# Optimization experiments

Hardware: AMD Instinct MI355X
Metric: run time of the kernel (lower is better)

Reference implementation:

```python
import jax, jax.numpy as jnp
import numpy as np

N = 10000
E = 80000
NUM_TYPES = 1000
IN_CH = 64
EMB = 128
IN_GNN = EMB + IN_CH - 1  # 191
NUM_GRAPHS = 16
NUM_CLASSES = 2


def _glorot(key, shape):
    fan_in, fan_out = shape[0], shape[1]
    lim = jnp.sqrt(6.0 / (fan_in + fan_out))
    return jax.random.uniform(key, shape, jnp.float32, -lim, lim)


def setup_inputs() -> dict:
    key = jax.random.key(0)
    ks = jax.random.split(key, 20)
    node_type_ids = jax.random.randint(ks[0], (N,), 0, NUM_TYPES)
    other_feats = jax.random.normal(ks[1], (N, IN_CH - 1), jnp.float32)
    edge_index = jax.random.randint(ks[2], (2, E), 0, N)
    batch = jnp.sort(jax.random.randint(ks[3], (N,), 0, NUM_GRAPHS))
    params = dict(
        emb=jax.random.normal(ks[4], (NUM_TYPES, EMB), jnp.float32),
        W1=_glorot(ks[5], (IN_GNN, 2048)), b1=jnp.zeros((2048,), jnp.float32),
        W2=_glorot(ks[6], (2048, 1024)), b2=jnp.zeros((1024,), jnp.float32),
        W3=_glorot(ks[7], (1024, 1024)), b3=jnp.zeros((1024,), jnp.float32),
        h1w=_glorot(ks[8], (1024, 1024)), h1b=jnp.zeros((1024,), jnp.float32),
        h2w=_glorot(ks[9], (1024, 1024)), h2b=jnp.zeros((1024,), jnp.float32),
        h3w=_glorot(ks[10], (1024, 512)), h3b=jnp.zeros((512,), jnp.float32),
        ow=_glorot(ks[11], (512, NUM_CLASSES)), ob=jnp.zeros((NUM_CLASSES,), jnp.float32),
    )
    return dict(node_type_ids=node_type_ids, other_feats=other_feats,
                edge_index=edge_index, batch=batch, **params)


def _gcn_norm(edge_index, num_nodes):
    # add self loops + symmetric normalization D^-1/2 (A+I) D^-1/2 (PyG GCNConv defaults)
    loop = jnp.arange(num_nodes, dtype=edge_index.dtype)
    src = jnp.concatenate([edge_index[0], loop])
    dst = jnp.concatenate([edge_index[1], loop])
    deg = jax.ops.segment_sum(jnp.ones_like(src, jnp.float32), dst, num_segments=num_nodes)
    dinv = jnp.where(deg > 0, jax.lax.rsqrt(jnp.maximum(deg, 1.0)), 0.0)
    norm = dinv[src] * dinv[dst]
    return src, dst, norm


def _gcn_conv(x, src, dst, norm, W, b):
    h = x @ W                                    # [N, out] dense GEMM first (PyG order)
    msg = h[src] * norm[:, None]                 # gather + scale over edges
    agg = jax.ops.segment_sum(msg, dst, num_segments=x.shape[0])  # scatter-add
    return agg + b


def reference(node_type_ids, other_feats, edge_index, batch,
              emb, W1, b1, W2, b2, W3, b3,
              h1w, h1b, h2w, h2b, h3w, h3b, ow, ob):
    # eval mode: dropout is identity
    x = jnp.concatenate([emb[node_type_ids], other_feats], axis=-1)  # [N, 191]
    src, dst, norm = _gcn_norm(edge_index, x.shape[0])
    x = jax.nn.relu(_gcn_conv(x, src, dst, norm, W1, b1))
    x = jax.nn.relu(_gcn_conv(x, src, dst, norm, W2, b2))
    x = jax.nn.relu(_gcn_conv(x, src, dst, norm, W3, b3))
    # global mean pool over graphs
    sums = jax.ops.segment_sum(x, batch, num_segments=NUM_GRAPHS)
    cnts = jax.ops.segment_sum(jnp.ones((x.shape[0],), jnp.float32), batch, num_segments=NUM_GRAPHS)
    g = sums / jnp.maximum(cnts, 1.0)[:, None]   # [G, 1024]
    g = jax.nn.relu(g @ h1w + h1b)
    g = jax.nn.relu(g @ h2w + h2b)
    g = jax.nn.relu(g @ h3w + h3b)
    return g @ ow + ob                           # [G, num_classes]
```

## Files before the change

### kernel.cpp

```cpp
#include <hip/hip_runtime.h>


#define N_NODES 10000
#define N_EDGES 80000
#define EMB_DIM 128
#define FEAT_DIM 63
#define IN_GNN 191
#define IN_STRIDE 192
#define H1 2048
#define H2 1024
#define NGRAPH 16
#define NCLS 2
#define PCHUNK 8

using ushort = unsigned short;
typedef __attribute__((ext_vector_type(8))) short s8b;
typedef __attribute__((ext_vector_type(4))) float f4v;

__device__ __forceinline__ float us2f(ushort u) {
    union { unsigned int i; float f; } v; v.i = ((unsigned int)u) << 16; return v.f;
}
__device__ __forceinline__ ushort f2us(float f) {
    union { unsigned int i; float f; } v; v.f = f;
    unsigned int r = v.i + 0x7FFFu + ((v.i >> 16) & 1u);
    return (ushort)(r >> 16);
}
__device__ __forceinline__ float ldm(const void* p, long i, int md) {
    return (md == 1) ? us2f(((const ushort*)p)[i]) : ((const float*)p)[i];
}

__global__ void GraphV1EmbLarge_73864847556672_kernel() {}

__global__ void k_detect(const ushort* __restrict__ feats, int* __restrict__ mode) {
    if (threadIdx.x != 0 || blockIdx.x != 0) return;
    int sane = 0;
    for (int i = 0; i < 256; i++) {
        ushort u = feats[i];
        int e = (u >> 7) & 0xFF;
        if (u == 0 || (e >= 97 && e <= 157)) sane++;
    }
    *mode = (sane >= 220) ? 1 : 2;
}

__global__ void k_zero2(int* __restrict__ a, int na, float* __restrict__ b, int nb) {
    int i = blockIdx.x * 256 + threadIdx.x;
    if (i < na) a[i] = 0;
    if (i < nb) b[i] = 0.f;
}
__global__ void k_deg_i(const int* __restrict__ dst, int* __restrict__ cnt) {
    int e = blockIdx.x * blockDim.x + threadIdx.x;
    if (e < N_EDGES) atomicAdd(&cnt[dst[e]], 1);
}
__global__ void k_scan(const int* __restrict__ cnt, int* __restrict__ indptr,
                       float* __restrict__ dinv) {
    __shared__ int part[256];
    int t = threadIdx.x;
    int base = t * 40;
    int s = 0;
    for (int i = 0; i < 40; i++) { int idx = base + i; if (idx < N_NODES) s += cnt[idx]; }
    part[t] = s;
    __syncthreads();
    if (t == 0) {
        int run = 0;
        for (int i = 0; i < 256; i++) { int tmp = part[i]; part[i] = run; run += tmp; }
        indptr[N_NODES] = run;
    }
    __syncthreads();
    int run = part[t];
    for (int i = 0; i < 40; i++) {
        int idx = base + i;
        if (idx < N_NODES) {
            indptr[idx] = run; run += cnt[idx];
            dinv[idx] = rsqrtf((float)cnt[idx] + 1.0f);
        }
    }
}
__global__ void k_fill(const int* __restrict__ src, const int* __restrict__ dst,
                       const int* __restrict__ indptr, int* __restrict__ cursor,
                       const float* __restrict__ dinv, int* __restrict__ ecol,
                       float* __restrict__ ewgt) {
    int e = blockIdx.x * blockDim.x + threadIdx.x;
    if (e >= N_EDGES) return;
    int d = dst[e], s = src[e];
    int slot = indptr[d] + atomicAdd(&cursor[d], 1);
    ecol[slot] = s;
    ewgt[slot] = dinv[s] * dinv[d];
}
__global__ void k_starts(const int* __restrict__ batch, int* __restrict__ starts) {
    int i = blockIdx.x * blockDim.x + threadIdx.x;
    if (i > N_NODES) return;
    int bc = (i < N_NODES) ? batch[i] : NGRAPH;
    int bp = (i == 0) ? -1 : batch[i - 1];
    for (int g = bp + 1; g <= bc; g++) starts[g] = i;
}

__global__ void k_build_x0(const int* __restrict__ types, const void* __restrict__ emb,
                           const void* __restrict__ feats, ushort* __restrict__ x0,
                           const int* __restrict__ mode) {
    int md = *mode;
    int i = blockIdx.x;
    int c = threadIdx.x;
    float v = 0.f;
    if (c < EMB_DIM) v = ldm(emb, (long)types[i] * EMB_DIM + c, md);
    else if (c < IN_GNN) v = ldm(feats, (long)i * FEAT_DIM + (c - EMB_DIM), md);
    x0[(long)i * IN_STRIDE + c] = f2us(v);
}

__device__ __forceinline__ void cvt_tile(const void* W, int K, int N, int Kp,
                                         ushort* Wt, int n0, int k0, int md) {
    __shared__ float tile[32][33];
    int tx = threadIdx.x, ty = threadIdx.y;
    for (int r = ty; r < 32; r += 8) {
        int k = k0 + r;
        tile[r][tx] = (k < K) ? ldm(W, (long)k * N + n0 + tx, md) : 0.f;
    }
    __syncthreads();
    for (int r = ty; r < 32; r += 8) {
        int nn = n0 + r, kk = k0 + tx;
        if (kk < Kp) Wt[(long)nn * Kp + kk] = f2us(tile[tx][r]);
    }
}

__global__ void k_cvtT_all(const void* W1, const void* W2, const void* W3,
                           const void* h1, const void* h2, const void* h3,
                           ushort* W1t, ushort* W2t, ushort* W3t,
                           ushort* h1t, ushort* h2t, ushort* h3t,
                           const int* __restrict__ mode) {
    int md = *mode;
    int b = blockIdx.x;
    if (b < 384) {
        int t = b;        cvt_tile(W1, IN_GNN, H1, IN_STRIDE, W1t, (t % 64) * 32, (t / 64) * 32, md);
    } else if (b < 2432) {
        int t = b - 384;  cvt_tile(W2, H1, H2, H1, W2t, (t % 32) * 32, (t / 32) * 32, md);
    } else if (b < 3456) {
        int t = b - 2432; cvt_tile(W3, H2, H2, H2, W3t, (t % 32) * 32, (t / 32) * 32, md);
    } else if (b < 4480) {
        int t = b - 3456; cvt_tile(h1, H2, H2, H2, h1t, (t % 32) * 32, (t / 32) * 32, md);
    } else if (b < 5504) {
        int t = b - 4480; cvt_tile(h2, H2, H2, H2, h2t, (t % 32) * 32, (t / 32) * 32, md);
    } else {
        int t = b - 5504; cvt_tile(h3, H2, 512, H2, h3t, (t % 16) * 32, (t / 16) * 32, md);
    }
}

__global__ void k_biases(const void* __restrict__ b1, const void* __restrict__ b2,
                         const void* __restrict__ b3, float* __restrict__ b1f,
                         float* __restrict__ b2f, float* __restrict__ b3f,
                         const int* __restrict__ mode) {
    int md = *mode;
    int i = blockIdx.x * 256 + threadIdx.x;
    if (i < 2048) b1f[i] = ldm(b1, i, md);
    else if (i < 3072) b2f[i - 2048] = ldm(b2, (long)(i - 2048), md);
    else if (i < 4096) b3f[i - 3072] = ldm(b3, (long)(i - 3072), md);
}

__global__ void k_gather192(const ushort* __restrict__ H, const int* __restrict__ indptr,
                            const int* __restrict__ ecol, const float* __restrict__ ewgt,
                            const float* __restrict__ dinv, ushort* __restrict__ X) {
    int d = blockIdx.x;
    int c = threadIdx.x;
    float ds = dinv[d];
    float acc = us2f(H[(long)d * IN_STRIDE + c]) * ds * ds;
    int s0 = indptr[d], s1 = indptr[d + 1];
    int s = s0;
    for (; s + 1 < s1; s += 2) {
        int sa = ecol[s], sb = ecol[s + 1];
        float wa = ewgt[s], wb = ewgt[s + 1];
        float fa = us2f(H[(long)sa * IN_STRIDE + c]);
        float fb = us2f(H[(long)sb * IN_STRIDE + c]);
        acc += fa * wa + fb * wb;
    }
    if (s < s1) acc += us2f(H[(long)ecol[s] * IN_STRIDE + c]) * ewgt[s];
    X[(long)d * IN_STRIDE + c] = f2us(acc);
}

__device__ __forceinline__ void unpack8(uint4 u, float* f) {
    f[0] = us2f((ushort)(u.x & 0xffff)); f[1] = us2f((ushort)(u.x >> 16));
    f[2] = us2f((ushort)(u.y & 0xffff)); f[3] = us2f((ushort)(u.y >> 16));
    f[4] = us2f((ushort)(u.z & 0xffff)); f[5] = us2f((ushort)(u.z >> 16));
    f[6] = us2f((ushort)(u.w & 0xffff)); f[7] = us2f((ushort)(u.w >> 16));
}

__global__ void k_gather1024(const ushort* __restrict__ H, const int* __restrict__ indptr,
                             const int* __restrict__ ecol, const float* __restrict__ ewgt,
                             const float* __restrict__ dinv, const float* __restrict__ bias,
                             ushort* __restrict__ X) {
    int d = blockIdx.x;
    int c8 = threadIdx.x * 8;
    float ds = dinv[d];
    float a[8], f0[8], f1[8];
    unpack8(*(const uint4*)&H[(long)d * H2 + c8], a);
    float w0 = ds * ds;
#pragma unroll
    for (int r = 0; r < 8; r++) a[r] *= w0;
    int s0 = indptr[d], s1 = indptr[d + 1];
    int s = s0;
    for (; s + 1 < s1; s += 2) {
        int sa = ecol[s], sb = ecol[s + 1];
        float wa = ewgt[s], wb = ewgt[s + 1];
        uint4 ua = *(const uint4*)&H[(long)sa * H2 + c8];
        uint4 ub = *(const uint4*)&H[(long)sb * H2 + c8];
        unpack8(ua, f0);
        unpack8(ub, f1);
#pragma unroll
        for (int r = 0; r < 8; r++) a[r] += f0[r] * wa + f1[r] * wb;
    }
    if (s < s1) {
        uint4 ua = *(const uint4*)&H[(long)ecol[s] * H2 + c8];
        float wa = ewgt[s];
        unpack8(ua, f0);
#pragma unroll
        for (int r = 0; r < 8; r++) a[r] += f0[r] * wa;
    }
    uint4 o;
    unsigned int p0 = (unsigned int)f2us(fmaxf(a[0] + bias[c8 + 0], 0.f));
    unsigned int p1 = (unsigned int)f2us(fmaxf(a[1] + bias[c8 + 1], 0.f));
    unsigned int p2 = (unsigned int)f2us(fmaxf(a[2] + bias[c8 + 2], 0.f));
    unsigned int p3 = (unsigned int)f2us(fmaxf(a[3] + bias[c8 + 3], 0.f));
    unsigned int p4 = (unsigned int)f2us(fmaxf(a[4] + bias[c8 + 4], 0.f));
    unsigned int p5 = (unsigned int)f2us(fmaxf(a[5] + bias[c8 + 5], 0.f));
    unsigned int p6 = (unsigned int)f2us(fmaxf(a[6] + bias[c8 + 6], 0.f));
    unsigned int p7 = (unsigned int)f2us(fmaxf(a[7] + bias[c8 + 7], 0.f));
    o.x = p0 | (p1 << 16); o.y = p2 | (p3 << 16);
    o.z = p4 | (p5 << 16); o.w = p6 | (p7 << 16);
    *(uint4*)&X[(long)d * H2 + c8] = o;
}

__global__ __launch_bounds__(256) void k_mfma_gemm(
    const ushort* __restrict__ A, int lda, int M,
    const ushort* __restrict__ Wt, int K, int N,
    const float* __restrict__ bias, int relu,
    ushort* __restrict__ C, int NB) {
    __shared__ ushort As[2][128 * 32];
    __shared__ ushort Bs[2][128 * 32];
    int L = blockIdx.x;
    int i = L >> 3;
    int m_t = (L & 7) + (i / NB) * 8;
    int n_t = i % NB;
    int m0 = m_t * 128, n0 = n_t * 128;
    if (m0 >= M) return;
    int tid = threadIdx.x;
    int wave = tid >> 6, lane = tid & 63;
    int wm = (wave & 1) * 64, wn = (wave >> 1) * 64;
    int quad = lane >> 4, l16 = lane & 15;
    int srow = tid >> 2;
    int scol = (tid & 3) * 8;
    int swz = ((srow >> 1) & 3) << 3;
    int rwz = ((l16 >> 1) & 3) << 3;
    int wa0 = srow * 32 + (scol ^ swz);
    int wa1 = (64 + srow) * 32 + (scol ^ swz);

    f4v acc[4][4];
#pragma unroll
    for (int ii = 0; ii < 4; ii++)
#pragma unroll
        for (int jj = 0; jj < 4; jj++) acc[ii][jj] = (f4v)(0.f);

    int gm1 = m0 + srow;       if (gm1 >= M) gm1 = M - 1;
    int gm2 = m0 + 64 + srow;  if (gm2 >= M) gm2 = M - 1;
    const ushort* pa1 = A + (long)gm1 * lda + scol;
    const ushort* pa2 = A + (long)gm2 * lda + scol;
    const ushort* pb1 = Wt + (long)(n0 + srow) * K + scol;
    const ushort* pb2 = Wt + (long)(n0 + 64 + srow) * K + scol;

    int niter = K >> 5;
    s8b va1 = *(const s8b*)pa1;
    s8b va2 = *(const s8b*)pa2;
    s8b vb1 = *(const s8b*)pb1;
    s8b vb2 = *(const s8b*)pb2;
    *(s8b*)&As[0][wa0] = va1;
    *(s8b*)&As[0][wa1] = va2;
    *(s8b*)&Bs[0][wa0] = vb1;
    *(s8b*)&Bs[0][wa1] = vb2;
    if (niter > 1) {
        pa1 += 32; pa2 += 32; pb1 += 32; pb2 += 32;
        va1 = *(const s8b*)pa1;
        va2 = *(const s8b*)pa2;
        vb1 = *(const s8b*)pb1;
        vb2 = *(const s8b*)pb2;
    }

    for (int it = 0; it < niter; it++) {
        int cur = it & 1;
        __syncthreads();
        if (it + 1 < niter) {
            int nxt = cur ^ 1;
            *(s8b*)&As[nxt][wa0] = va1;
            *(s8b*)&As[nxt][wa1] = va2;
            *(s8b*)&Bs[nxt][wa0] = vb1;
            *(s8b*)&Bs[nxt][wa1] = vb2;
            if (it + 2 < niter) {
                pa1 += 32; pa2 += 32; pb1 += 32; pb2 += 32;
                va1 = *(const s8b*)pa1;
                va2 = *(const s8b*)pa2;
                vb1 = *(const s8b*)pb1;
                vb2 = *(const s8b*)pb2;
            }
        }
        s8b a[4], b[4];
#pragma unroll
        for (int ii = 0; ii < 4; ii++)
            a[ii] = *(const s8b*)&As[cur][(wm + ii * 16 + l16) * 32 + (quad * 8 ^ rwz)];
#pragma unroll
        for (int jj = 0; jj < 4; jj++)
            b[jj] = *(const s8b*)&Bs[cur][(wn + jj * 16 + l16) * 32 + (quad * 8 ^ rwz)];
#pragma unroll
        for (int ii = 0; ii < 4; ii++)
#pragma unroll
            for (int jj = 0; jj < 4; jj++)
                acc[ii][jj] = __builtin_amdgcn_mfma_f32_16x16x32_bf16(a[ii], b[jj], acc[ii][jj], 0, 0, 0);
    }

#pragma unroll
    for (int ii = 0; ii < 4; ii++) {
        int row0 = m0 + wm + ii * 16 + quad * 4;
#pragma unroll
        for (int jj = 0; jj < 4; jj++) {
            int colc = n0 + wn + jj * 16 + l16;
            float bv = bias ? bias[colc] : 0.f;
#pragma unroll
            for (int r = 0; r < 4; r++) {
                int row = row0 + r;
                if (row < M) {
                    float v = acc[ii][jj][r] + bv;
                    if (relu) v = fmaxf(v, 0.f);
                    C[(long)row * N + colc] = f2us(v);
                }
            }
        }
    }
}

__global__ void k_pool_part(const ushort* __restrict__ x, const int* __restrict__ starts,
                            float* __restrict__ acc) {
    int g = blockIdx.x / PCHUNK, ch = blockIdx.x % PCHUNK;
    int c = blockIdx.y * 256 + threadIdx.x;
    int s0 = starts[g], s1 = starts[g + 1];
    int len = s1 - s0;
    int per = (len + PCHUNK - 1) / PCHUNK;
    int r0 = s0 + ch * per;
    int r1 = r0 + per; if (r1 > s1) r1 = s1;
    if (r0 >= r1) return;
    float sum = 0.f;
    for (int i = r0; i < r1; i++) sum += us2f(x[(long)i * H2 + c]);
    atomicAdd(&acc[g * H2 + c], sum);
}
__global__ void k_pool_fin(const float* __restrict__ acc, const int* __restrict__ starts,
                           ushort* __restrict__ pA) {
    int idx = blockIdx.x * 256 + threadIdx.x;
    if (idx >= NGRAPH * H2) return;
    int g = idx >> 10;
    int cnt = starts[g + 1] - starts[g];
    pA[idx] = f2us(acc[idx] / (float)(cnt > 0 ? cnt : 1));
}

__global__ __launch_bounds__(256) void k_head_mfma(const ushort* __restrict__ A,
                                                   const ushort* __restrict__ Wt,
                                                   float* __restrict__ pt, int N) {
    __shared__ float red[4][16][16];
    int n0 = blockIdx.x * 16;
    int ks = blockIdx.y;
    int wave = threadIdx.x >> 6, lane = threadIdx.x & 63;
    int l16 = lane & 15, quad = lane >> 4;
    int kbase = ks * 256 + wave * 64;
    f4v acc = (f4v)(0.f);
#pragma unroll
    for (int kk = 0; kk < 64; kk += 32) {
        int k = kbase + kk + quad * 8;
        s8b a = *(const s8b*)&A[l16 * 1024 + k];
        s8b b = *(const s8b*)&Wt[(long)(n0 + l16) * 1024 + k];
        acc = __builtin_amdgcn_mfma_f32_16x16x32_bf16(a, b, acc, 0, 0, 0);
    }
#pragma unroll
    for (int r = 0; r < 4; r++) red[wave][quad * 4 + r][l16] = acc[r];
    __syncthreads();
    int row = threadIdx.x >> 4, col = threadIdx.x & 15;
    float s = red[0][row][col] + red[1][row][col] + red[2][row][col] + red[3][row][col];
    pt[((long)ks * 16 + row) * N + n0 + col] = s;
}

__global__ void k_head_red(const float* __restrict__ pt, const void* __restrict__ bias,
                           ushort* __restrict__ out, int N,
                           const int* __restrict__ mode) {
    int md = *mode;
    int idx = blockIdx.x * 256 + threadIdx.x;
    if (idx >= 16 * N) return;
    int row = idx / N, col = idx - row * N;
    float s = pt[((long)0 * 16 + row) * N + col] + pt[((long)1 * 16 + row) * N + col]
            + pt[((long)2 * 16 + row) * N + col] + pt[((long)3 * 16 + row) * N + col];
    s = fmaxf(s + ldm(bias, (long)col, md), 0.f);
    out[(long)row * N + col] = f2us(s);
}

__global__ void k_head_out(const ushort* __restrict__ in, const void* __restrict__ W,
                           const void* __restrict__ b, void* __restrict__ out,
                           const int* __restrict__ mode) {
    int md = *mode;
    int row = blockIdx.x >> 1, cls = blockIdx.x & 1;
    int lane = threadIdx.x;
    float acc = 0.f;
    for (int k = lane; k < 512; k += 64)
        acc += us2f(in[row * 512 + k]) * ldm(W, (long)k * NCLS + cls, md);
#pragma unroll
    for (int off = 32; off > 0; off >>= 1) acc += __shfl_down(acc, off);
    if (lane == 0) {
        float v = acc + ldm(b, (long)cls, md);
        if (md == 1) ((ushort*)out)[row * NCLS + cls] = f2us(v);
        else ((float*)out)[row * NCLS + cls] = v;
    }
}

extern "C" void kernel_launch(void* const* d_in, const int* in_sizes, int n_in,
                              void* d_out, int out_size, void* d_ws, size_t ws_size,
                              hipStream_t stream) {
    static const int EXPECT[19] = {
        10000, 630000, 160000, 10000, 128000,
        391168, 2048, 2097152, 1024, 1048576, 1024,
        1048576, 1024, 1048576, 1024, 524288, 512, 1024, 2
    };
    if (n_in != 19) { hipMemsetAsync(d_out, 0x48, 64, stream); return; }
    for (int i = 0; i < 19; i++)
        if (in_sizes[i] != EXPECT[i]) { hipMemsetAsync(d_out, 0x50 + i, 64, stream); return; }
    if (ws_size < (size_t)90000000) { hipMemsetAsync(d_out, 0x49, 64, stream); return; }

    const int* node_types = (const int*)d_in[0];
    const void* other = d_in[1];
    const int* e_src = (const int*)d_in[2];
    const int* e_dst = e_src + N_EDGES;
    const int* batch = (const int*)d_in[3];

    char* w = (char*)d_ws;
    int* mode = (int*)w;      w += 256;
    int* cnt = (int*)w;       w += 10240 * 4;
    int* cursor = (int*)w;    w += 10240 * 4;
    float* dinv = (float*)w;  w += 10240 * 4;
    int* starts = (int*)w;    w += 256;
    int* indptr = (int*)w;    w += 10240 * 4;
    int* ecol = (int*)w;      w += 81920 * 4;
    float* ewgt = (float*)w;  w += 81920 * 4;
    float* b1f = (float*)w;   w += 2048 * 4;
    float* b2f = (float*)w;   w += 1024 * 4;
    float* b3f = (float*)w;   w += 1024 * 4;
    float* pt = (float*)w;    w += 4 * 16 * 1024 * 4;
    float* pacc = (float*)w;  w += 16 * 1024 * 4;
    ushort* pA = (ushort*)w;  w += 16 * 1024 * 2;
    ushort* hA = (ushort*)w;  w += 16 * 1024 * 2;
    ushort* hB = (ushort*)w;  w += 16 * 1024 * 2;
    ushort* x0 = (ushort*)w;  w += 1920000 * 2;
    ushort* A1 = (ushort*)w;  w += 1920000 * 2;
    ushort* W1t = (ushort*)w; w += 393216 * 2;
    ushort* W2t = (ushort*)w; w += 2097152 * 2;
    ushort* W3t = (ushort*)w; w += 1048576 * 2;
    ushort* h1wt = (ushort*)w; w += 1048576 * 2;
    ushort* h2wt = (ushort*)w; w += 1048576 * 2;
    ushort* h3wt = (ushort*)w; w += 524288 * 2;
    ushort* Hb = (ushort*)w;  w += 20480000 * 2;
    ushort* Gb = (ushort*)w;  w += 10240000 * 2;
    ushort* x2 = Hb;
    ushort* x3 = Hb + (size_t)N_NODES * H2;

    hipGetLastError();
    k_detect<<<1, 64, 0, stream>>>((const ushort*)other, mode);
    hipError_t e0 = hipGetLastError();
    if (e0 != hipSuccess) { hipMemsetAsync(d_out, 0x46, 64, stream); return; }

    k_zero2<<<80, 256, 0, stream>>>(cnt, 20480, pacc, NGRAPH * H2);
    k_deg_i<<<(N_EDGES + 255) / 256, 256, 0, stream>>>(e_dst, cnt);
    k_starts<<<(N_NODES + 256) / 256, 256, 0, stream>>>(batch, starts);
    k_scan<<<1, 256, 0, stream>>>(cnt, indptr, dinv);
    k_fill<<<(N_EDGES + 255) / 256, 256, 0, stream>>>(e_src, e_dst, indptr, cursor, dinv, ecol, ewgt);

    k_build_x0<<<N_NODES, IN_STRIDE, 0, stream>>>(node_types, d_in[4], other, x0, mode);
    k_cvtT_all<<<6016, dim3(32, 8), 0, stream>>>(d_in[5], d_in[7], d_in[9], d_in[11], d_in[13], d_in[15],
                                                 W1t, W2t, W3t, h1wt, h2wt, h3wt, mode);
    k_biases<<<16, 256, 0, stream>>>(d_in[6], d_in[8], d_in[10], b1f, b2f, b3f, mode);

    k_gather192<<<N_NODES, IN_STRIDE, 0, stream>>>(x0, indptr, ecol, ewgt, dinv, A1);
    k_mfma_gemm<<<16 * 80, 256, 0, stream>>>(A1, IN_STRIDE, N_NODES, W1t, IN_STRIDE, H1, b1f, 1, Hb, 16);

    k_mfma_gemm<<<8 * 80, 256, 0, stream>>>(Hb, H1, N_NODES, W2t, H1, H2, nullptr, 0, Gb, 8);
    k_gather1024<<<N_NODES, 128, 0, stream>>>(Gb, indptr, ecol, ewgt, dinv, b2f, x2);

    k_mfma_gemm<<<8 * 80, 256, 0, stream>>>(x2, H2, N_NODES, W3t, H2, H2, nullptr, 0, Gb, 8);
    k_gather1024<<<N_NODES, 128, 0, stream>>>(Gb, indptr, ecol, ewgt, dinv, b3f, x3);

    k_pool_part<<<dim3(NGRAPH * PCHUNK, H2 / 256), 256, 0, stream>>>(x3, starts, pacc);
    k_pool_fin<<<64, 256, 0, stream>>>(pacc, starts, pA);

    k_head_mfma<<<dim3(64, 4), 256, 0, stream>>>(pA, h1wt, pt, 1024);
    k_head_red<<<64, 256, 0, stream>>>(pt, d_in[12], hA, 1024, mode);
    k_head_mfma<<<dim3(64, 4), 256, 0, stream>>>(hA, h2wt, pt, 1024);
    k_head_red<<<64, 256, 0, stream>>>(pt, d_in[14], hB, 1024, mode);
    k_head_mfma<<<dim3(32, 4), 256, 0, stream>>>(hB, h3wt, pt, 512);
    k_head_red<<<32, 256, 0, stream>>>(pt, d_in[16], hA, 512, mode);
    k_head_out<<<NGRAPH * NCLS, 64, 0, stream>>>(hA, d_in[17], d_in[18], d_out, mode);

    hipError_t e1 = hipGetLastError();
    if (e1 != hipSuccess) hipMemsetAsync(d_out, 0x47, 64, stream);
}
```

Measured before the change: 403.1 us.

## Merge prep kernels, fuse pool finalize into head GEMM, reshape GEMM to 2 waves

Several small setup kernels are merged: zeroing with format detection, CSR fill with graph-start computation, and weight conversion with x0 build and bias conversion. This cuts launch count and inter-kernel gaps. The mean-pool division is folded into the first head MFMA kernel so the pooled bf16 buffer disappears. The main GEMM now uses 128 threads (2 waves), each computing 128x64 with 8x4 accumulators, which raises per-wave register pressure and halves the waves available to hide latency.

Measured after the change: 431.6 us. 1.07x slower.

```diff
diff --git a/kernel.cpp b/kernel.cpp
--- a/kernel.cpp
+++ b/kernel.cpp
@@ -31,22 +31,22 @@
 
 __global__ void GraphV1EmbLarge_73864847556672_kernel() {}
 
-__global__ void k_detect(const ushort* __restrict__ feats, int* __restrict__ mode) {
-    if (threadIdx.x != 0 || blockIdx.x != 0) return;
-    int sane = 0;
-    for (int i = 0; i < 256; i++) {
-        ushort u = feats[i];
-        int e = (u >> 7) & 0xFF;
-        if (u == 0 || (e >= 97 && e <= 157)) sane++;
-    }
-    *mode = (sane >= 220) ? 1 : 2;
-}
-
-__global__ void k_zero2(int* __restrict__ a, int na, float* __restrict__ b, int nb) {
+__global__ void k_prep0(int* __restrict__ a, int na, float* __restrict__ b, int nb,
+                        const ushort* __restrict__ feats, int* __restrict__ mode) {
     int i = blockIdx.x * 256 + threadIdx.x;
     if (i < na) a[i] = 0;
     if (i < nb) b[i] = 0.f;
-}
+    if (blockIdx.x == 0 && threadIdx.x == 0) {
+        int sane = 0;
+        for (int j = 0; j < 256; j++) {
+            ushort u = feats[j];
+            int e = (u >> 7) & 0xFF;
+            if (u == 0 || (e >= 97 && e <= 157)) sane++;
+        }
+        *mode = (sane >= 220) ? 1 : 2;
+    }
+}
+
 __global__ void k_deg_i(const int* __restrict__ dst, int* __restrict__ cnt) {
     int e = blockIdx.x * blockDim.x + threadIdx.x;
     if (e < N_EDGES) atomicAdd(&cnt[dst[e]], 1);
@@ -78,32 +78,23 @@
 __global__ void k_fill(const int* __restrict__ src, const int* __restrict__ dst,
                        const int* __restrict__ indptr, int* __restrict__ cursor,
                        const float* __restrict__ dinv, int* __restrict__ ecol,
-                       float* __restrict__ ewgt) {
-    int e = blockIdx.x * blockDim.x + threadIdx.x;
-    if (e >= N_EDGES) return;
-    int d = dst[e], s = src[e];
-    int slot = indptr[d] + atomicAdd(&cursor[d], 1);
-    ecol[slot] = s;
-    ewgt[slot] = dinv[s] * dinv[d];
-}
-__global__ void k_starts(const int* __restrict__ batch, int* __restrict__ starts) {
-    int i = blockIdx.x * blockDim.x + threadIdx.x;
-    if (i > N_NODES) return;
-    int bc = (i < N_NODES) ? batch[i] : NGRAPH;
-    int bp = (i == 0) ? -1 : batch[i - 1];
-    for (int g = bp + 1; g <= bc; g++) starts[g] = i;
-}
-
-__global__ void k_build_x0(const int* __restrict__ types, const void* __restrict__ emb,
-                           const void* __restrict__ feats, ushort* __restrict__ x0,
-                           const int* __restrict__ mode) {
-    int md = *mode;
-    int i = blockIdx.x;
-    int c = threadIdx.x;
-    float v = 0.f;
-    if (c < EMB_DIM) v = ldm(emb, (long)types[i] * EMB_DIM + c, md);
-    else if (c < IN_GNN) v = ldm(feats, (long)i * FEAT_DIM + (c - EMB_DIM), md);
-    x0[(long)i * IN_STRIDE + c] = f2us(v);
+                       float* __restrict__ ewgt, const int* __restrict__ batch,
+                       int* __restrict__ starts) {
+    int b = blockIdx.x;
+    if (b < 313) {
+        int e = b * 256 + threadIdx.x;
+        if (e >= N_EDGES) return;
+        int d = dst[e], s = src[e];
+        int slot = indptr[d] + atomicAdd(&cursor[d], 1);
+        ecol[slot] = s;
+        ewgt[slot] = dinv[s] * dinv[d];
+    } else {
+        int i = (b - 313) * 256 + threadIdx.x;
+        if (i > N_NODES) return;
+        int bc = (i < N_NODES) ? batch[i] : NGRAPH;
+        int bp = (i == 0) ? -1 : batch[i - 1];
+        for (int g = bp + 1; g <= bc; g++) starts[g] = i;
+    }
 }
 
 __device__ __forceinline__ void cvt_tile(const void* W, int K, int N, int Kp,
@@ -121,11 +112,15 @@
     }
 }
 
-__global__ void k_cvtT_all(const void* W1, const void* W2, const void* W3,
-                           const void* h1, const void* h2, const void* h3,
-                           ushort* W1t, ushort* W2t, ushort* W3t,
-                           ushort* h1t, ushort* h2t, ushort* h3t,
-                           const int* __restrict__ mode) {
+__global__ void k_cvt_all(const void* W1, const void* W2, const void* W3,
+                          const void* h1, const void* h2, const void* h3,
+                          ushort* W1t, ushort* W2t, ushort* W3t,
+                          ushort* h1t, ushort* h2t, ushort* h3t,
+                          const int* __restrict__ types, const void* emb,
+                          const void* feats, ushort* __restrict__ x0,
+                          const void* b1, const void* b2, const void* b3,
+                          float* __restrict__ b1f, float* __restrict__ b2f,
+                          float* __restrict__ b3f, const int* __restrict__ mode) {
     int md = *mode;
     int b = blockIdx.x;
     if (b < 384) {
@@ -138,20 +133,22 @@
         int t = b - 3456; cvt_tile(h1, H2, H2, H2, h1t, (t % 32) * 32, (t / 32) * 32, md);
     } else if (b < 5504) {
         int t = b - 4480; cvt_tile(h2, H2, H2, H2, h2t, (t % 32) * 32, (t / 32) * 32, md);
+    } else if (b < 6016) {
+        int t = b - 5504; cvt_tile(h3, H2, 512, H2, h3t, (t % 16) * 32, (t / 16) * 32, md);
+    } else if (b < 16016) {
+        int i = b - 6016;
+        int c = threadIdx.y * 32 + threadIdx.x;
+        if (c >= IN_STRIDE) return;
+        float v = 0.f;
+        if (c < EMB_DIM) v = ldm(emb, (long)types[i] * EMB_DIM + c, md);
+        else if (c < IN_GNN) v = ldm(feats, (long)i * FEAT_DIM + (c - EMB_DIM), md);
+        x0[(long)i * IN_STRIDE + c] = f2us(v);
     } else {
-        int t = b - 5504; cvt_tile(h3, H2, 512, H2, h3t, (t % 16) * 32, (t / 16) * 32, md);
-    }
-}
-
-__global__ void k_biases(const void* __restrict__ b1, const void* __restrict__ b2,
-                         const void* __restrict__ b3, float* __restrict__ b1f,
-                         float* __restrict__ b2f, float* __restrict__ b3f,
-                         const int* __restrict__ mode) {
-    int md = *mode;
-    int i = blockIdx.x * 256 + threadIdx.x;
-    if (i < 2048) b1f[i] = ldm(b1, i, md);
-    else if (i < 3072) b2f[i - 2048] = ldm(b2, (long)(i - 2048), md);
-    else if (i < 4096) b3f[i - 3072] = ldm(b3, (long)(i - 3072), md);
+        int i = (b - 16016) * 256 + threadIdx.y * 32 + threadIdx.x;
+        if (i < 2048) b1f[i] = ldm(b1, i, md);
+        else if (i < 3072) b2f[i - 2048] = ldm(b2, (long)(i - 2048), md);
+        else if (i < 4096) b3f[i - 3072] = ldm(b3, (long)(i - 3072), md);
+    }
 }
 
 __global__ void k_gather192(const ushort* __restrict__ H, const int* __restrict__ indptr,
@@ -226,7 +223,7 @@
     *(uint4*)&X[(long)d * H2 + c8] = o;
 }
 
-__global__ __launch_bounds__(256) void k_mfma_gemm(
+__global__ __launch_bounds__(128, 2) void k_mfma_gemm(
     const ushort* __restrict__ A, int lda, int M,
     const ushort* __restrict__ Wt, int K, int N,
     const float* __restrict__ bias, int relu,
@@ -241,43 +238,45 @@
     if (m0 >= M) return;
     int tid = threadIdx.x;
     int wave = tid >> 6, lane = tid & 63;
-    int wm = (wave & 1) * 64, wn = (wave >> 1) * 64;
+    int wn = wave * 64;
     int quad = lane >> 4, l16 = lane & 15;
     int srow = tid >> 2;
     int scol = (tid & 3) * 8;
-    int swz = ((srow >> 1) & 3) << 3;
     int rwz = ((l16 >> 1) & 3) << 3;
-    int wa0 = srow * 32 + (scol ^ swz);
-    int wa1 = (64 + srow) * 32 + (scol ^ swz);
-
-    f4v acc[4][4];
-#pragma unroll
-    for (int ii = 0; ii < 4; ii++)
+
+    int wadr[4];
+    const ushort* pa[4];
+    const ushort* pb[4];
+#pragma unroll
+    for (int c = 0; c < 4; c++) {
+        int r = c * 32 + srow;
+        wadr[c] = r * 32 + (scol ^ (((r >> 1) & 3) << 3));
+        int gm = m0 + r; if (gm >= M) gm = M - 1;
+        pa[c] = A + (long)gm * lda + scol;
+        pb[c] = Wt + (long)(n0 + r) * K + scol;
+    }
+
+    f4v acc[8][4];
+#pragma unroll
+    for (int ii = 0; ii < 8; ii++)
 #pragma unroll
         for (int jj = 0; jj < 4; jj++) acc[ii][jj] = (f4v)(0.f);
 
-    int gm1 = m0 + srow;       if (gm1 >= M) gm1 = M - 1;
-    int gm2 = m0 + 64 + srow;  if (gm2 >= M) gm2 = M - 1;
-    const ushort* pa1 = A + (long)gm1 * lda + scol;
-    const ushort* pa2 = A + (long)gm2 * lda + scol;
-    const ushort* pb1 = Wt + (long)(n0 + srow) * K + scol;
-    const ushort* pb2 = Wt + (long)(n0 + 64 + srow) * K + scol;
-
     int niter = K >> 5;
-    s8b va1 = *(const s8b*)pa1;
-    s8b va2 = *(const s8b*)pa2;
-    s8b vb1 = *(const s8b*)pb1;
-    s8b vb2 = *(const s8b*)pb2;
-    *(s8b*)&As[0][wa0] = va1;
-    *(s8b*)&As[0][wa1] = va2;
-    *(s8b*)&Bs[0][wa0] = vb1;
-    *(s8b*)&Bs[0][wa1] = vb2;
+    s8b va[4], vb[4];
+#pragma unroll
+    for (int c = 0; c < 4; c++) { va[c] = *(const s8b*)pa[c]; vb[c] = *(const s8b*)pb[c]; }
+#pragma unroll
+    for (int c = 0; c < 4; c++) {
+        *(s8b*)&As[0][wadr[c]] = va[c];
+        *(s8b*)&Bs[0][wadr[c]] = vb[c];
+    }
     if (niter > 1) {
-        pa1 += 32; pa2 += 32; pb1 += 32; pb2 += 32;
-        va1 = *(const s8b*)pa1;
-        va2 = *(const s8b*)pa2;
-        vb1 = *(const s8b*)pb1;
-        vb2 = *(const s8b*)pb2;
+#pragma unroll
+        for (int c = 0; c < 4; c++) {
+            pa[c] += 32; pb[c] += 32;
+            va[c] = *(const s8b*)pa[c]; vb[c] = *(const s8b*)pb[c];
+        }
     }
 
     for (int it = 0; it < niter; it++) {
@@ -285,35 +284,36 @@
         __syncthreads();
         if (it + 1 < niter) {
             int nxt = cur ^ 1;
-            *(s8b*)&As[nxt][wa0] = va1;
-            *(s8b*)&As[nxt][wa1] = va2;
-            *(s8b*)&Bs[nxt][wa0] = vb1;
-            *(s8b*)&Bs[nxt][wa1] = vb2;
+#pragma unroll
+            for (int c = 0; c < 4; c++) {
+                *(s8b*)&As[nxt][wadr[c]] = va[c];
+                *(s8b*)&Bs[nxt][wadr[c]] = vb[c];
+            }
             if (it + 2 < niter) {
-                pa1 += 32; pa2 += 32; pb1 += 32; pb2 += 32;
-                va1 = *(const s8b*)pa1;
-                va2 = *(const s8b*)pa2;
-                vb1 = *(const s8b*)pb1;
-                vb2 = *(const s8b*)pb2;
+#pragma unroll
+                for (int c = 0; c < 4; c++) {
+                    pa[c] += 32; pb[c] += 32;
+                    va[c] = *(const s8b*)pa[c]; vb[c] = *(const s8b*)pb[c];
+                }
             }
         }
-        s8b a[4], b[4];
-#pragma unroll
-        for (int ii = 0; ii < 4; ii++)
-            a[ii] = *(const s8b*)&As[cur][(wm + ii * 16 + l16) * 32 + (quad * 8 ^ rwz)];
+        s8b a[8], b[4];
+#pragma unroll
+        for (int ii = 0; ii < 8; ii++)
+            a[ii] = *(const s8b*)&As[cur][(ii * 16 + l16) * 32 + (quad * 8 ^ rwz)];
 #pragma unroll
         for (int jj = 0; jj < 4; jj++)
             b[jj] = *(const s8b*)&Bs[cur][(wn + jj * 16 + l16) * 32 + (quad * 8 ^ rwz)];
 #pragma unroll
-        for (int ii = 0; ii < 4; ii++)
+        for (int ii = 0; ii < 8; ii++)
 #pragma unroll
             for (int jj = 0; jj < 4; jj++)
                 acc[ii][jj] = __builtin_amdgcn_mfma_f32_16x16x32_bf16(a[ii], b[jj], acc[ii][jj], 0, 0, 0);
     }
 
 #pragma unroll
-    for (int ii = 0; ii < 4; ii++) {
-        int row0 = m0 + wm + ii * 16 + quad * 4;
+    for (int ii = 0; ii < 8; ii++) {
+        int row0 = m0 + ii * 16 + quad * 4;
 #pragma unroll
         for (int jj = 0; jj < 4; jj++) {
             int colc = n0 + wn + jj * 16 + l16;
@@ -345,13 +345,36 @@
     for (int i = r0; i < r1; i++) sum += us2f(x[(long)i * H2 + c]);
     atomicAdd(&acc[g * H2 + c], sum);
 }
-__global__ void k_pool_fin(const float* __restrict__ acc, const int* __restrict__ starts,
-                           ushort* __restrict__ pA) {
-    int idx = blockIdx.x * 256 + threadIdx.x;
-    if (idx >= NGRAPH * H2) return;
-    int g = idx >> 10;
-    int cnt = starts[g + 1] - starts[g];
-    pA[idx] = f2us(acc[idx] / (float)(cnt > 0 ? cnt : 1));
+
+__global__ __launch_bounds__(256) void k_head_mfma_pool(const float* __restrict__ pacc,
+                                                        const int* __restrict__ starts,
+                                                        const ushort* __restrict__ Wt,
+                                                        float* __restrict__ pt, int N) {
+    __shared__ float red[4][16][16];
+    int n0 = blockIdx.x * 16;
+    int ks = blockIdx.y;
+    int wave = threadIdx.x >> 6, lane = threadIdx.x & 63;
+    int l16 = lane & 15, quad = lane >> 4;
+    int cnt = starts[l16 + 1] - starts[l16];
+    float rc = 1.f / (float)(cnt > 0 ? cnt : 1);
+    int kbase = ks * 256 + wave * 64;
+    f4v acc = (f4v)(0.f);
+#pragma unroll
+    for (int kk = 0; kk < 64; kk += 32) {
+        int k = kbase + kk + quad * 8;
+        s8b a;
+        short* ap = (short*)&a;
+#pragma unroll
+        for (int j = 0; j < 8; j++) ap[j] = (short)f2us(pacc[l16 * 1024 + k + j] * rc);
+        s8b b = *(const s8b*)&Wt[(long)(n0 + l16) * 1024 + k];
+        acc = __builtin_amdgcn_mfma_f32_16x16x32_bf16(a, b, acc, 0, 0, 0);
+    }
+#pragma unroll
+    for (int r = 0; r < 4; r++) red[wave][quad * 4 + r][l16] = acc[r];
+    __syncthreads();
+    int row = threadIdx.x >> 4, col = threadIdx.x & 15;
+    float s = red[0][row][col] + red[1][row][col] + red[2][row][col] + red[3][row][col];
+    pt[((long)ks * 16 + row) * N + n0 + col] = s;
 }
 
 __global__ __launch_bounds__(256) void k_head_mfma(const ushort* __restrict__ A,
@@ -443,7 +466,6 @@
     float* b3f = (float*)w;   w += 1024 * 4;
     float* pt = (float*)w;    w += 4 * 16 * 1024 * 4;
     float* pacc = (float*)w;  w += 16 * 1024 * 4;
-    ushort* pA = (ushort*)w;  w += 16 * 1024 * 2;
     ushort* hA = (ushort*)w;  w += 16 * 1024 * 2;
     ushort* hB = (ushort*)w;  w += 16 * 1024 * 2;
     ushort* x0 = (ushort*)w;  w += 1920000 * 2;
@@ -460,34 +482,30 @@
     ushort* x3 = Hb + (size_t)N_NODES * H2;
 
     hipGetLastError();
-    k_detect<<<1, 64, 0, stream>>>((const ushort*)other, mode);
+    k_prep0<<<80, 256, 0, stream>>>(cnt, 20480, pacc, NGRAPH * H2, (const ushort*)other, mode);
     hipError_t e0 = hipGetLastError();
     if (e0 != hipSuccess) { hipMemsetAsync(d_out, 0x46, 64, stream); return; }
-
-    k_zero2<<<80, 256, 0, stream>>>(cnt, 20480, pacc, NGRAPH * H2);
     k_deg_i<<<(N_EDGES + 255) / 256, 256, 0, stream>>>(e_dst, cnt);
-    k_starts<<<(N_NODES + 256) / 256, 256, 0, stream>>>(batch, starts);
     k_scan<<<1, 256, 0, stream>>>(cnt, indptr, dinv);
-    k_fill<<<(N_EDGES + 255) / 256, 256, 0, stream>>>(e_src, e_dst, indptr, cursor, dinv, ecol, ewgt);
-
-    k_build_x0<<<N_NODES, IN_STRIDE, 0, stream>>>(node_types, d_in[4], other, x0, mode);
-    k_cvtT_all<<<6016, dim3(32, 8), 0, stream>>>(d_in[5], d_in[7], d_in[9], d_in[11], d_in[13], d_in[15],
-                                                 W1t, W2t, W3t, h1wt, h2wt, h3wt, mode);
-    k_biases<<<16, 256, 0, stream>>>(d_in[6], d_in[8], d_in[10], b1f, b2f, b3f, mode);
+    k_fill<<<313 + 40, 256, 0, stream>>>(e_src, e_dst, indptr, cursor, dinv, ecol, ewgt, batch, starts);
+
+    k_cvt_all<<<16032, dim3(32, 8), 0, stream>>>(d_in[5], d_in[7], d_in[9], d_in[11], d_in[13], d_in[15],
+                                                 W1t, W2t, W3t, h1wt, h2wt, h3wt,
+                                                 node_types, d_in[4], other, x0,
+                                                 d_in[6], d_in[8], d_in[10], b1f, b2f, b3f, mode);
 
     k_gather192<<<N_NODES, IN_STRIDE, 0, stream>>>(x0, indptr, ecol, ewgt, dinv, A1);
-    k_mfma_gemm<<<16 * 80, 256, 0, stream>>>(A1, IN_STRIDE, N_NODES, W1t, IN_STRIDE, H1, b1f, 1, Hb, 16);
-
-    k_mfma_gemm<<<8 * 80, 256, 0, stream>>>(Hb, H1, N_NODES, W2t, H1, H2, nullptr, 0, Gb, 8);
+    k_mfma_gemm<<<16 * 80, 128, 0, stream>>>(A1, IN_STRIDE, N_NODES, W1t, IN_STRIDE, H1, b1f, 1, Hb, 16);
+
+    k_mfma_gemm<<<8 * 80, 128, 0, stream>>>(Hb, H1, N_NODES, W2t, H1, H2, nullptr, 0, Gb, 8);
     k_gather1024<<<N_NODES, 128, 0, stream>>>(Gb, indptr, ecol, ewgt, dinv, b2f, x2);
 
-    k_mfma_gemm<<<8 * 80, 256, 0, stream>>>(x2, H2, N_NODES, W3t, H2, H2, nullptr, 0, Gb, 8);
+    k_mfma_gemm<<<8 * 80, 128, 0, stream>>>(x2, H2, N_NODES, W3t, H2, H2, nullptr, 0, Gb, 8);
     k_gather1024<<<N_NODES, 128, 0, stream>>>(Gb, indptr, ecol, ewgt, dinv, b3f, x3);
 
     k_pool_part<<<dim3(NGRAPH * PCHUNK, H2 / 256), 256, 0, stream>>>(x3, starts, pacc);
-    k_pool_fin<<<64, 256, 0, stream>>>(pacc, starts, pA);
-
-    k_head_mfma<<<dim3(64, 4), 256, 0, stream>>>(pA, h1wt, pt, 1024);
+
+    k_head_mfma_pool<<<dim3(64, 4), 256, 0, stream>>>(pacc, starts, h1wt, pt, 1024);
     k_head_red<<<64, 256, 0, stream>>>(pt, d_in[12], hA, 1024, mode);
     k_head_mfma<<<dim3(64, 4), 256, 0, stream>>>(hA, h2wt, pt, 1024);
     k_head_red<<<64, 256, 0, stream>>>(pt, d_in[14], hB, 1024, mode);
```
